# Optimization experiments

Measured on AMD Instinct MI355X. Metric: run time of the kernel, lower is better.

The kernel has to match this reference:

```python
import jax, jax.numpy as jnp
import numpy as np

# ---- static configuration (mirrors init_kwargs) ----
B, NCAM = 1, 6
FC, FH, FW = 128, 16, 44              # featureShape
ORFH, ORFW = 128, 352                 # transformedImgShape H, W
D_ST, D_END, D_STEP = 1.0, 49.0, 1.0
D = int(np.arange(D_ST, D_END, D_STEP).shape[0])   # 48 depth bins
OUTC = 128
XB = (-50.0, 50.0, 1.0)
YB = (-50.0, 50.0, 1.0)
BEV_H = int((YB[1] - YB[0]) / YB[2])  # 100
BEV_W = int((XB[1] - XB[0]) / XB[2])  # 100
THRESH = 0.05                         # opacity_filter
ERR_TOL = 1.0                         # error_tolerance
COV_DILATE = 0.3                      # 3DGS low-pass on 2D cov diagonal
ALPHA_MAX = 0.99
ALPHA_MIN = 1.0 / 255.0
BN_EPS = 1e-3


def _frustum():
    ds = jnp.arange(D_ST, D_END, D_STEP, dtype=jnp.float32)[:, None, None]
    xs = jnp.linspace(0.0, ORFW - 1.0, FW, dtype=jnp.float32)[None, None, :]
    ys = jnp.linspace(0.0, ORFH - 1.0, FH, dtype=jnp.float32)[None, :, None]
    shp = (D, FH, FW)
    return jnp.stack([jnp.broadcast_to(xs, shp), jnp.broadcast_to(ys, shp),
                      jnp.broadcast_to(ds, shp)], axis=-1)  # [D,FH,FW,3]


def _conv(x, w, b, pad):
    y = jax.lax.conv_general_dilated(x, w, (1, 1), [(pad, pad), (pad, pad)],
                                     dimension_numbers=('NCHW', 'OIHW', 'NCHW'))
    return y + b[None, :, None, None]


def _bn(x, g, beta, m, v):
    # eval-mode BatchNorm2d with running stats
    inv = g / jnp.sqrt(v + BN_EPS)
    return (x - m[None, :, None, None]) * inv[None, :, None, None] + beta[None, :, None, None]


def _rasterize(features, means, cov6, opac):
    """Differentiable BEV Gaussian splatting (alpha compositing in index order).
    features [G,C], means [G,3] (normalized to [-1,1]), cov6 [G,6]=(xx,xy,xz,yy,yz,zz), opac [G].
    """
    h, w = BEV_H, BEV_W
    sh, sw = h / 2.0, w / 2.0                 # h/FoVy, w/FoVx with FoV=2
    op = jnp.where(opac > THRESH, opac, 0.0)  # opacity cull (variable-length mask in torch)
    # full_proj_transform: row0 -> row index (y), row1 -> col index (x)
    py = h / 2.0 - sh * means[:, 1]
    px = w / 2.0 - sw * means[:, 0]
    # 2D covariance in (py,px) basis: J Sigma3 J^T with J = [[0,-sh,0],[-sw,0,0]]
    a = sh * sh * cov6[:, 3] + COV_DILATE     # var along py (from Sigma_yy)
    b = sh * sw * cov6[:, 1]                  # cov(py,px) (from Sigma_xy)
    c = sw * sw * cov6[:, 0] + COV_DILATE     # var along px (from Sigma_xx)
    det = a * c - b * b
    op = jnp.where(det > 0.0, op, 0.0)
    inv_det = 1.0 / jnp.where(det > 0.0, det, 1.0)
    ys = jnp.arange(h, dtype=jnp.float32)
    xs = jnp.arange(w, dtype=jnp.float32)
    dy = py[None, :] - ys[:, None]            # [h,G]
    dx = px[None, :] - xs[:, None]            # [w,G]
    # power = -0.5 d^T Sigma2^{-1} d, Sigma2^{-1} = [[c,-b],[-b,a]]/det
    power = (-0.5 * (c * inv_det) * dy * dy)[:, None, :] \
            + (-0.5 * (a * inv_det) * dx * dx)[None, :, :] \
            + (b * inv_det) * dy[:, None, :] * dx[None, :, :]   # [h,w,G]
    alpha = jnp.minimum(ALPHA_MAX, op * jnp.exp(jnp.minimum(power, 0.0)))
    alpha = jnp.where(alpha < ALPHA_MIN, 0.0, alpha)
    T = jnp.cumprod(1.0 - alpha, axis=-1)
    T_excl = jnp.concatenate([jnp.ones_like(T[..., :1]), T[..., :-1]], axis=-1)
    wgt = alpha * T_excl                      # [h,w,G]
    bev = jnp.einsum('hwg,gc->chw', wgt, features)   # bg color = 0
    return bev


def reference(cam2ego_rot, cam2ego_trans, cam_intrins, post_cam2ego_rot, post_cam2ego_trans,
              img_feats, conv1_w, conv1_b, bn1_g, bn1_b, bn1_m, bn1_v,
              conv2_w, conv2_b, bn2_g, bn2_b, bn2_m, bn2_v, conv3_w, conv3_b):
    # --- geometry lifting ---
    frustum = _frustum()                                             # [D,FH,FW,3]
    pts = frustum[None, None] - post_cam2ego_trans[:, :, None, None, None, :]
    pts = jnp.einsum('bnij,bndhwj->bndhwi', jnp.linalg.inv(post_cam2ego_rot), pts)
    pts = jnp.concatenate([pts[..., :2] * pts[..., 2:3], pts[..., 2:3]], axis=-1)
    combine = cam2ego_rot @ jnp.linalg.inv(cam_intrins)
    geometry = jnp.einsum('bnij,bndhwj->bndhwi', combine, pts) \
               + cam2ego_trans[:, :, None, None, None, :]            # [B,N,D,FH,FW,3]
    # --- depth net ---
    x = img_feats.reshape(B * NCAM, FC, FH, FW)
    x = jax.nn.relu(_bn(_conv(x, conv1_w, conv1_b, 1), bn1_g, bn1_b, bn1_m, bn1_v))
    x = jax.nn.relu(_bn(_conv(x, conv2_w, conv2_b, 1), bn2_g, bn2_b, bn2_m, bn2_v))
    x = _conv(x, conv3_w, conv3_b, 0)                                # [B*N, OUTC+D+1, H, W]
    depth_prob = jax.nn.softmax(x[:, :D], axis=1).reshape(B, NCAM, D, FH, FW)
    opac = jax.nn.sigmoid(x[:, D:D + 1]).reshape(B, NCAM, FH, FW)
    feats = x[:, D + 1:].reshape(B, NCAM, OUTC, FH, FW)
    # --- per-pixel Gaussian moments over the depth distribution ---
    means3d = jnp.einsum('bndhw,bndhwi->bnhwi', depth_prob, geometry)
    delta = means3d[:, :, None] - geometry                           # [B,N,D,FH,FW,3]
    cov = jnp.einsum('bndhw,bndhwi,bndhwj->bnhwij', depth_prob, delta, delta)
    cov = cov * (ERR_TOL ** 2 / 9.0)
    # --- normalize to BEV frame ---
    center = jnp.array([(XB[0] + XB[1]) / 2.0, (YB[0] + YB[1]) / 2.0, 0.0], jnp.float32)
    scale = jnp.array([2.0 / (XB[1] - XB[0]), 2.0 / (YB[1] - YB[0]), 1.0], jnp.float32)
    means_n = (means3d - center) * scale
    cov_n = cov * (scale[:, None] * scale[None, :])
    cov6 = jnp.stack([cov_n[..., 0, 0], cov_n[..., 0, 1], cov_n[..., 0, 2],
                      cov_n[..., 1, 1], cov_n[..., 1, 2], cov_n[..., 2, 2]], axis=-1)
    G = NCAM * FH * FW
    f = jnp.transpose(feats, (0, 1, 3, 4, 2)).reshape(B, G, OUTC)
    m = means_n.reshape(B, G, 3)
    c6 = cov6.reshape(B, G, 6)
    o = opac.reshape(B, G)
    bev = jax.vmap(_rasterize)(f, m, c6, o)                          # [B,OUTC,BEV_H,BEV_W]
    return bev


def setup_inputs() -> dict:
    key = jax.random.key(0)
    ks = jax.random.split(key, 16)
    eye = jnp.eye(3, dtype=jnp.float32)
    cam2ego_rot = eye + 0.05 * jax.random.normal(ks[0], (B, NCAM, 3, 3), jnp.float32)
    cam2ego_trans = 0.5 * jax.random.normal(ks[1], (B, NCAM, 3), jnp.float32)
    intr = jnp.array([[260.0, 0.0, ORFW / 2.0], [0.0, 260.0, ORFH / 2.0], [0.0, 0.0, 1.0]], jnp.float32)
    cam_intrins = jnp.broadcast_to(intr, (B, NCAM, 3, 3)) * (1.0 + 0.01 * jax.random.normal(ks[2], (B, NCAM, 1, 1), jnp.float32))
    post_cam2ego_rot = eye + 0.01 * jax.random.normal(ks[3], (B, NCAM, 3, 3), jnp.float32)
    post_cam2ego_trans = 2.0 * jax.random.normal(ks[4], (B, NCAM, 3), jnp.float32)
    img_feats = jax.random.normal(ks[5], (B, NCAM, FC, FH, FW), jnp.float32)
    def cw(k, o, i, kh, kw):
        return jax.random.normal(k, (o, i, kh, kw), jnp.float32) / np.sqrt(i * kh * kw)
    inp = dict(cam2ego_rot=cam2ego_rot, cam2ego_trans=cam2ego_trans, cam_intrins=cam_intrins,
               post_cam2ego_rot=post_cam2ego_rot, post_cam2ego_trans=post_cam2ego_trans,
               img_feats=img_feats,
               conv1_w=cw(ks[6], FC, FC, 3, 3), conv1_b=jnp.zeros((FC,), jnp.float32),
               bn1_g=jnp.ones((FC,), jnp.float32), bn1_b=0.1 * jax.random.normal(ks[7], (FC,), jnp.float32),
               bn1_m=jnp.zeros((FC,), jnp.float32), bn1_v=jnp.ones((FC,), jnp.float32),
               conv2_w=cw(ks[8], FC, FC, 3, 3), conv2_b=jnp.zeros((FC,), jnp.float32),
               bn2_g=jnp.ones((FC,), jnp.float32), bn2_b=0.1 * jax.random.normal(ks[9], (FC,), jnp.float32),
               bn2_m=jnp.zeros((FC,), jnp.float32), bn2_v=jnp.ones((FC,), jnp.float32),
               conv3_w=cw(ks[10], OUTC + D + 1, FC, 1, 1),
               conv3_b=jnp.zeros((OUTC + D + 1,), jnp.float32))
    return inp
```

## Files before the change

kernel.cpp:

```cpp
#include <hip/hip_runtime.h>
#include <math.h>

#define NCAM 6
#define FHh 16
#define FWw 44
#define PIX 704
#define FCc 128
#define DB 48
#define C3 177
#define C3PAD 192
#define KCONV 1152
#define NG 4224
#define BEVN 10000
#define NSPLIT 3
#define SG 1408
#define TH_LOG (-5.5412635f)

#define OFF_WT1    0
#define OFF_WT2    147456
#define OFF_WT3    294912
#define OFF_GEO    319488
#define OFF_X1     724992
#define OFF_X2     1265664
#define OFF_X3     1806336
#define OFF_PART   2553984
#define OFF_PRM    4716672
#define OFF_PRM2   4733568
#define OFF_FEATT  4742016
#define OFF_SF     0
#define OFF_SP     3840000

typedef __attribute__((ext_vector_type(8))) short bf16x8;
typedef __attribute__((ext_vector_type(4))) float f32x4;
typedef __attribute__((ext_vector_type(4))) int i32x4;

__device__ __forceinline__ unsigned short f2bf(float x) {
  unsigned u = __float_as_uint(x);
  return (unsigned short)((u + 0x7FFF + ((u >> 16) & 1)) >> 16);
}
__device__ __forceinline__ float bf2f(unsigned short h) {
  return __uint_as_float(((unsigned)h) << 16);
}

__device__ __forceinline__ void inv3(const float* A, float* I) {
  float a=A[0],b=A[1],c=A[2],d=A[3],e=A[4],f=A[5],g=A[6],h=A[7],i=A[8];
  float c0 = e*i - f*h, c1 = f*g - d*i, c2 = d*h - e*g;
  float det = a*c0 + b*c1 + c*c2;
  float id = 1.f/det;
  I[0]=c0*id; I[1]=(c*h-b*i)*id; I[2]=(b*f-c*e)*id;
  I[3]=c1*id; I[4]=(a*i-c*g)*id; I[5]=(c*d-a*f)*id;
  I[6]=c2*id; I[7]=(b*g-a*h)*id; I[8]=(a*e-b*d)*id;
}

__global__ void k_prep(const float* __restrict__ rot, const float* __restrict__ intr,
                       const float* __restrict__ post_rot,
                       const float* __restrict__ trans, const float* __restrict__ post_trans,
                       const float* __restrict__ w1, const float* __restrict__ w2,
                       const float* __restrict__ w3, float* __restrict__ ws) {
  if (blockIdx.x < 792) {
    __shared__ float sm[NCAM][24];
    if (threadIdx.x < NCAM) {
      int n = threadIdx.x;
      float ip[9], ii[9];
      inv3(post_rot + n*9, ip);
      inv3(intr + n*9, ii);
      const float* R = rot + n*9;
      for (int j = 0; j < 9; ++j) sm[n][j] = ip[j];
      for (int r = 0; r < 3; ++r)
        for (int c = 0; c < 3; ++c) {
          float s = 0.f;
          for (int k = 0; k < 3; ++k) s += R[r*3+k]*ii[k*3+c];
          sm[n][9 + r*3 + c] = s;
        }
    }
    __syncthreads();
    int idx = blockIdx.x*256 + threadIdx.x;
    if (idx >= NCAM*DB*PIX) return;
    int n = idx / (DB*PIX);
    int rem = idx % (DB*PIX);
    int d = rem / PIX;
    int hw = rem % PIX;
    int h = hw / FWw, w = hw % FWw;
    float fx = w * (351.0f/43.0f);
    float fy = h * (127.0f/15.0f);
    float fz = 1.0f + (float)d;
    const float* pt = post_trans + n*3;
    float v0 = fx - pt[0], v1 = fy - pt[1], v2 = fz - pt[2];
    const float* m = sm[n];
    float x = m[0]*v0 + m[1]*v1 + m[2]*v2;
    float y = m[3]*v0 + m[4]*v1 + m[5]*v2;
    float z = m[6]*v0 + m[7]*v1 + m[8]*v2;
    float q0 = x*z, q1 = y*z, q2 = z;
    const float* c = m + 9;
    const float* t = trans + n*3;
    float gx = c[0]*q0 + c[1]*q1 + c[2]*q2 + t[0];
    float gy = c[3]*q0 + c[4]*q1 + c[5]*q2 + t[1];
    ((float2*)(ws + OFF_GEO))[idx] = make_float2(gx, gy);
  } else {
    int e = (blockIdx.x - 792)*256 + threadIdx.x;
    if (e < 147456) {
      float v1 = w1[e], v2 = w2[e];
      unsigned short h1 = f2bf(v1), h2 = f2bf(v2);
      unsigned short l1 = f2bf(v1 - bf2f(h1)), l2 = f2bf(v2 - bf2f(h2));
      unsigned short* wt1 = (unsigned short*)(ws + OFF_WT1);
      unsigned short* wt2 = (unsigned short*)(ws + OFF_WT2);
      wt1[e] = h1; wt1[147456 + e] = l1;
      wt2[e] = h2; wt2[147456 + e] = l2;
    }
    if (e < 192*128) {
      int oc = e >> 7, k = e & 127;
      float v = (oc < C3) ? w3[oc*FCc + k] : 0.f;
      unsigned short h = f2bf(v);
      unsigned short* wt3 = (unsigned short*)(ws + OFF_WT3);
      wt3[e] = h; wt3[24576 + e] = f2bf(v - bf2f(h));
    }
  }
}

#define LROW 20

__global__ __launch_bounds__(256) void k_gemm_mfma(
    const float* __restrict__ in, const float* ws, float* __restrict__ part, int woff)
{
  __shared__ int alds[2][64*LROW];
  __shared__ int blds[2][64*LROW];
  int tid = threadIdx.x;
  int px0 = blockIdx.x * 64;
  int oc0 = blockIdx.y * 64;
  int z = blockIdx.z; int n = z >> 2, ks = z & 3;
  const unsigned short* whi = (const unsigned short*)(ws + woff);
  const unsigned short* wlo = whi + 147456;
  const float* inn = in + (size_t)n*FCc*PIX;
  int wv = tid >> 6, lane = tid & 63;
  int a_oc = tid >> 2, a_kq = tid & 3;
  int b_px = tid & 63, b_kq = tid >> 6;
  int p = px0 + b_px; int b_y = p / FWw, b_x = p - b_y*FWw;
  int k00 = ks * 288;

  i32x4 pa_h, pa_l; float bv[8];
  auto issueA = [&](int s) {
    size_t gi = (size_t)(oc0 + a_oc)*KCONV + (k00 + s*32 + a_kq*8);
    pa_h = *(const i32x4*)(whi + gi);
    pa_l = *(const i32x4*)(wlo + gi);
  };
  auto issueB = [&](int s) {
    #pragma unroll
    for (int j = 0; j < 8; ++j) {
      int k = k00 + s*32 + b_kq*8 + j;
      int ic = k / 9, tap = k - ic*9;
      int ky = tap / 3, kx = tap - ky*3;
      int yy = b_y + ky - 1, xx = b_x + kx - 1;
      float v = 0.f;
      if ((unsigned)yy < FHh && (unsigned)xx < FWw) v = inn[(size_t)ic*PIX + yy*FWw + xx];
      bv[j] = v;
    }
  };

  f32x4 a00 = {0.f,0.f,0.f,0.f}, a01 = a00, a10 = a00, a11 = a00;
  int ocr = (wv >> 1) * 32, pxr = (wv & 1) * 32;
  int dq = (lane >> 4) * 4;
  int rA0 = (ocr + (lane & 15)) * LROW + dq;
  int rA1 = rA0 + 16*LROW;
  int rB0 = (pxr + (lane & 15)) * LROW + dq;
  int rB1 = rB0 + 16*LROW;
  int aw = a_oc*LROW + a_kq*4;
  int bw = b_px*LROW + b_kq*4;

  issueA(0); issueB(0);
  for (int s = 0; s < 9; ++s) {
    __syncthreads();
    *(i32x4*)&alds[0][aw] = pa_h;
    *(i32x4*)&alds[1][aw] = pa_l;
    {
      i32x4 vh, vl;
      int th[8], tl[8];
      #pragma unroll
      for (int j = 0; j < 8; ++j) {
        unsigned short h = f2bf(bv[j]);
        th[j] = h; tl[j] = f2bf(bv[j] - bf2f(h));
      }
      vh.x = th[0]|(th[1]<<16); vh.y = th[2]|(th[3]<<16);
      vh.z = th[4]|(th[5]<<16); vh.w = th[6]|(th[7]<<16);
      vl.x = tl[0]|(tl[1]<<16); vl.y = tl[2]|(tl[3]<<16);
      vl.z = tl[4]|(tl[5]<<16); vl.w = tl[6]|(tl[7]<<16);
      *(i32x4*)&blds[0][bw] = vh;
      *(i32x4*)&blds[1][bw] = vl;
    }
    __syncthreads();
    if (s < 8) { issueA(s+1); issueB(s+1); }
    bf16x8 ah0 = *(bf16x8*)&alds[0][rA0], ah1 = *(bf16x8*)&alds[0][rA1];
    bf16x8 al0 = *(bf16x8*)&alds[1][rA0], al1 = *(bf16x8*)&alds[1][rA1];
    bf16x8 bh0 = *(bf16x8*)&blds[0][rB0], bh1 = *(bf16x8*)&blds[0][rB1];
    bf16x8 bl0 = *(bf16x8*)&blds[1][rB0], bl1 = *(bf16x8*)&blds[1][rB1];
    a00 = __builtin_amdgcn_mfma_f32_16x16x32_bf16(ah0, bh0, a00, 0, 0, 0);
    a01 = __builtin_amdgcn_mfma_f32_16x16x32_bf16(ah0, bh1, a01, 0, 0, 0);
    a10 = __builtin_amdgcn_mfma_f32_16x16x32_bf16(ah1, bh0, a10, 0, 0, 0);
    a11 = __builtin_amdgcn_mfma_f32_16x16x32_bf16(ah1, bh1, a11, 0, 0, 0);
    a00 = __builtin_amdgcn_mfma_f32_16x16x32_bf16(ah0, bl0, a00, 0, 0, 0);
    a01 = __builtin_amdgcn_mfma_f32_16x16x32_bf16(ah0, bl1, a01, 0, 0, 0);
    a10 = __builtin_amdgcn_mfma_f32_16x16x32_bf16(ah1, bl0, a10, 0, 0, 0);
    a11 = __builtin_amdgcn_mfma_f32_16x16x32_bf16(ah1, bl1, a11, 0, 0, 0);
    a00 = __builtin_amdgcn_mfma_f32_16x16x32_bf16(al0, bh0, a00, 0, 0, 0);
    a01 = __builtin_amdgcn_mfma_f32_16x16x32_bf16(al0, bh1, a01, 0, 0, 0);
    a10 = __builtin_amdgcn_mfma_f32_16x16x32_bf16(al1, bh0, a10, 0, 0, 0);
    a11 = __builtin_amdgcn_mfma_f32_16x16x32_bf16(al1, bh1, a11, 0, 0, 0);
  }
  float* pp = part + (size_t)(ks*NCAM + n)*FCc*PIX;
  int ocb = oc0 + ocr + ((lane >> 4) << 2);
  int pxb = px0 + pxr + (lane & 15);
  #pragma unroll
  for (int i = 0; i < 4; ++i) {
    pp[(size_t)(ocb + i)*PIX + pxb]           = a00[i];
    pp[(size_t)(ocb + i)*PIX + pxb + 16]      = a01[i];
    pp[(size_t)(ocb + 16 + i)*PIX + pxb]      = a10[i];
    pp[(size_t)(ocb + 16 + i)*PIX + pxb + 16] = a11[i];
  }
}

__global__ __launch_bounds__(256) void k_gemm_mfma3(
    const float* __restrict__ in, const float* ws,
    const float* __restrict__ bias, float* __restrict__ outbuf)
{
  __shared__ int alds[2][64*LROW];
  __shared__ int blds[2][64*LROW];
  int tid = threadIdx.x;
  int px0 = blockIdx.x * 64;
  int oc0 = blockIdx.y * 64;
  int n = blockIdx.z;
  const unsigned short* whi = (const unsigned short*)(ws + OFF_WT3);
  const unsigned short* wlo = whi + 24576;
  const float* inn = in + (size_t)n*FCc*PIX;
  int wv = tid >> 6, lane = tid & 63;
  int a_oc = tid >> 2, a_kq = tid & 3;
  int b_px = tid & 63, b_kq = tid >> 6;
  int p = px0 + b_px;

  i32x4 pa_h, pa_l; float bvv[8];
  auto issueA = [&](int s) {
    size_t gi = (size_t)(oc0 + a_oc)*128 + (s*32 + a_kq*8);
    pa_h = *(const i32x4*)(whi + gi);
    pa_l = *(const i32x4*)(wlo + gi);
  };
  auto issueB = [&](int s) {
    #pragma unroll
    for (int j = 0; j < 8; ++j) {
      int ic = s*32 + b_kq*8 + j;
      bvv[j] = inn[(size_t)ic*PIX + p];
    }
  };

  f32x4 a00 = {0.f,0.f,0.f,0.f}, a01 = a00, a10 = a00, a11 = a00;
  int ocr = (wv >> 1) * 32, pxr = (wv & 1) * 32;
  int dq = (lane >> 4) * 4;
  int rA0 = (ocr + (lane & 15)) * LROW + dq;
  int rA1 = rA0 + 16*LROW;
  int rB0 = (pxr + (lane & 15)) * LROW + dq;
  int rB1 = rB0 + 16*LROW;
  int aw = a_oc*LROW + a_kq*4;
  int bw = b_px*LROW + b_kq*4;

  issueA(0); issueB(0);
  for (int s = 0; s < 4; ++s) {
    __syncthreads();
    *(i32x4*)&alds[0][aw] = pa_h;
    *(i32x4*)&alds[1][aw] = pa_l;
    {
      i32x4 vh, vl;
      int th[8], tl[8];
      #pragma unroll
      for (int j = 0; j < 8; ++j) {
        unsigned short h = f2bf(bvv[j]);
        th[j] = h; tl[j] = f2bf(bvv[j] - bf2f(h));
      }
      vh.x = th[0]|(th[1]<<16); vh.y = th[2]|(th[3]<<16);
      vh.z = th[4]|(th[5]<<16); vh.w = th[6]|(th[7]<<16);
      vl.x = tl[0]|(tl[1]<<16); vl.y = tl[2]|(tl[3]<<16);
      vl.z = tl[4]|(tl[5]<<16); vl.w = tl[6]|(tl[7]<<16);
      *(i32x4*)&blds[0][bw] = vh;
      *(i32x4*)&blds[1][bw] = vl;
    }
    __syncthreads();
    if (s < 3) { issueA(s+1); issueB(s+1); }
    bf16x8 ah0 = *(bf16x8*)&alds[0][rA0], ah1 = *(bf16x8*)&alds[0][rA1];
    bf16x8 al0 = *(bf16x8*)&alds[1][rA0], al1 = *(bf16x8*)&alds[1][rA1];
    bf16x8 bh0 = *(bf16x8*)&blds[0][rB0], bh1 = *(bf16x8*)&blds[0][rB1];
    bf16x8 bl0 = *(bf16x8*)&blds[1][rB0], bl1 = *(bf16x8*)&blds[1][rB1];
    a00 = __builtin_amdgcn_mfma_f32_16x16x32_bf16(ah0, bh0, a00, 0, 0, 0);
    a01 = __builtin_amdgcn_mfma_f32_16x16x32_bf16(ah0, bh1, a01, 0, 0, 0);
    a10 = __builtin_amdgcn_mfma_f32_16x16x32_bf16(ah1, bh0, a10, 0, 0, 0);
    a11 = __builtin_amdgcn_mfma_f32_16x16x32_bf16(ah1, bh1, a11, 0, 0, 0);
    a00 = __builtin_amdgcn_mfma_f32_16x16x32_bf16(ah0, bl0, a00, 0, 0, 0);
    a01 = __builtin_amdgcn_mfma_f32_16x16x32_bf16(ah0, bl1, a01, 0, 0, 0);
    a10 = __builtin_amdgcn_mfma_f32_16x16x32_bf16(ah1, bl0, a10, 0, 0, 0);
    a11 = __builtin_amdgcn_mfma_f32_16x16x32_bf16(ah1, bl1, a11, 0, 0, 0);
    a00 = __builtin_amdgcn_mfma_f32_16x16x32_bf16(al0, bh0, a00, 0, 0, 0);
    a01 = __builtin_amdgcn_mfma_f32_16x16x32_bf16(al0, bh1, a01, 0, 0, 0);
    a10 = __builtin_amdgcn_mfma_f32_16x16x32_bf16(al1, bh0, a10, 0, 0, 0);
    a11 = __builtin_amdgcn_mfma_f32_16x16x32_bf16(al1, bh1, a11, 0, 0, 0);
  }
  int ocb = oc0 + ocr + ((lane >> 4) << 2);
  int pxb = px0 + pxr + (lane & 15);
  #pragma unroll
  for (int i = 0; i < 4; ++i) {
    int o0 = ocb + i, o1 = ocb + 16 + i;
    if (o0 < C3) {
      float b = bias[o0];
      outbuf[(size_t)(n*C3 + o0)*PIX + pxb]      = a00[i] + b;
      outbuf[(size_t)(n*C3 + o0)*PIX + pxb + 16] = a01[i] + b;
    }
    if (o1 < C3) {
      float b = bias[o1];
      outbuf[(size_t)(n*C3 + o1)*PIX + pxb]      = a10[i] + b;
      outbuf[(size_t)(n*C3 + o1)*PIX + pxb + 16] = a11[i] + b;
    }
  }
}

__global__ void k_epi_bn(const float* __restrict__ part, const float* __restrict__ cb,
                         const float* __restrict__ g, const float* __restrict__ be,
                         const float* __restrict__ mn, const float* __restrict__ vr,
                         float* __restrict__ out, int KSPLIT)
{
  int idx = blockIdx.x*256 + threadIdx.x;
  if (idx >= NCAM*FCc*176) return;
  int px4 = idx % 176;
  int t = idx / 176;
  int oc = t % FCc;
  int n = t / FCc;
  float4 s = {0.f,0.f,0.f,0.f};
  for (int ks = 0; ks < KSPLIT; ++ks) {
    const float4* p = (const float4*)(part + (size_t)((ks*NCAM+n)*FCc + oc)*PIX);
    float4 v = p[px4];
    s.x += v.x; s.y += v.y; s.z += v.z; s.w += v.w;
  }
  float inv = g[oc] * rsqrtf(vr[oc] + 1e-3f);
  float sh = (cb[oc] - mn[oc]) * inv + be[oc];
  float4 o;
  o.x = fmaxf(s.x*inv + sh, 0.f);
  o.y = fmaxf(s.y*inv + sh, 0.f);
  o.z = fmaxf(s.z*inv + sh, 0.f);
  o.w = fmaxf(s.w*inv + sh, 0.f);
  ((float4*)(out + (size_t)(n*FCc + oc)*PIX))[px4] = o;
}

__global__ void k_moments(float* __restrict__ ws) {
  int wid  = (blockIdx.x * 256 + threadIdx.x) >> 6;
  int lane = threadIdx.x & 63;
  int n = wid / PIX, hw = wid % PIX;
  const float* x3 = ws + OFF_X3 + (size_t)n*C3*PIX + hw;
  float logit = (lane < DB) ? x3[(size_t)lane*PIX] : -1e30f;
  float mx = logit;
  for (int off = 1; off < 64; off <<= 1) mx = fmaxf(mx, __shfl_xor(mx, off));
  float e = (lane < DB) ? expf(logit - mx) : 0.f;
  float s = e;
  for (int off = 1; off < 64; off <<= 1) s += __shfl_xor(s, off);
  float p = e / s;
  float gx = 0.f, gy = 0.f;
  if (lane < DB) {
    float2 g2 = ((const float2*)(ws + OFF_GEO))[(size_t)(n*DB + lane)*PIX + hw];
    gx = g2.x; gy = g2.y;
  }
  float sx = p*gx;
  for (int off = 1; off < 64; off <<= 1) sx += __shfl_xor(sx, off);
  float sy = p*gy;
  for (int off = 1; off < 64; off <<= 1) sy += __shfl_xor(sy, off);
  float dx = gx - sx, dy = gy - sy;
  float c00 = p*dx*dx, c01 = p*dx*dy, c11 = p*dy*dy;
  for (int off = 1; off < 64; off <<= 1) c00 += __shfl_xor(c00, off);
  for (int off = 1; off < 64; off <<= 1) c01 += __shfl_xor(c01, off);
  for (int off = 1; off < 64; off <<= 1) c11 += __shfl_xor(c11, off);
  float opl = x3[(size_t)DB*PIX];
  float opac = 1.f / (1.f + expf(-opl));
  float a = c11*(1.f/9.f) + 0.3f;
  float b = c01*(1.f/9.f);
  float c = c00*(1.f/9.f) + 0.3f;
  float py = 50.f - sy;
  float px = 50.f - sx;
  float det = a*c - b*b;
  float op = (opac > 0.05f) ? opac : 0.f;
  float invd = 1.f;
  if (det > 0.f) invd = 1.f/det; else op = 0.f;
  if (lane == 0) {
    float lop = (op > 0.f) ? logf(op) : -1e30f;
    ((float4*)(ws + OFF_PRM))[wid]  = make_float4(py, px, -0.5f*c*invd, -0.5f*a*invd);
    ((float2*)(ws + OFF_PRM2))[wid] = make_float2(b*invd, lop);
  }
  unsigned lo = f2bf(x3[(size_t)(DB + 1 + 2*lane)*PIX]);
  unsigned hi = f2bf(x3[(size_t)(DB + 1 + 2*lane + 1)*PIX]);
  ((unsigned*)(ws + OFF_FEATT))[(size_t)wid*64 + lane] = lo | (hi << 16);
}

template<int CTRL, int RMASK>
__device__ __forceinline__ float dpp_mul(float v) {
  int t = __builtin_amdgcn_update_dpp(0x3f800000, __float_as_int(v), CTRL, RMASK, 0xF, false);
  return v * __int_as_float(t);
}

__global__ __launch_bounds__(1024) void k_raster(const float* __restrict__ ws,
                                                 float* __restrict__ wsout) {
  __shared__ float4 s4[SG];
  __shared__ float2 s2[SG];
  int lane = threadIdx.x & 63, wv = threadIdx.x >> 6;
  int split = blockIdx.x / 625;
  int pxb   = blockIdx.x % 625;
  int pix = pxb * 16 + wv;
  float yi = (float)(pix / 100), xi = (float)(pix % 100);
  int gbase = split * SG;
  const float4* prm4 = (const float4*)(ws + OFF_PRM) + gbase;
  const float2* prm2 = (const float2*)(ws + OFF_PRM2) + gbase;
  const unsigned* ftu = (const unsigned*)(ws + OFF_FEATT);
  for (int i = threadIdx.x; i < SG; i += 1024) {
    s4[i] = prm4[i];
    s2[i] = prm2[i];
  }
  __syncthreads();
  float T = 1.f, ax = 0.f, ay = 0.f;
  for (int gl = 0; gl < SG; gl += 64) {
    float4 c4 = s4[gl + lane];
    float2 c2 = s2[gl + lane];
    float dyv = c4.x - yi, dxv = c4.y - xi;
    float pw = c4.z*dyv*dyv + c4.w*dxv*dxv + c2.x*dyv*dxv;
    float t  = pw + c2.y;
    bool hit = (t >= TH_LOG);
    unsigned long long m0 = __ballot(hit);
    if (m0) {
      float alpha = __expf(fminf(t, c2.y));
      alpha = fminf(alpha, 0.99f);
      alpha = hit ? alpha : 0.f;
      float P = 1.f - alpha;
      P = dpp_mul<0x111, 0xF>(P);
      P = dpp_mul<0x112, 0xF>(P);
      P = dpp_mul<0x114, 0xF>(P);
      P = dpp_mul<0x118, 0xF>(P);
      P = dpp_mul<0x142, 0xA>(P);
      P = dpp_mul<0x143, 0xC>(P);
      float E = __int_as_float(__builtin_amdgcn_update_dpp(
                  0x3f800000, __float_as_int(P), 0x138, 0xF, 0xF, false));
      float w = alpha * T * E;
      T *= __int_as_float(__builtin_amdgcn_readlane(__float_as_int(P), 63));
      unsigned long long mask = __ballot(w > 1e-9f);
      int g0 = gbase + gl;
      while (mask) {
        int jj[8];
        #pragma unroll
        for (int b = 0; b < 8; ++b) {
          if (mask) { jj[b] = __builtin_ctzll(mask); mask &= mask - 1ull; }
          else jj[b] = -1;
        }
        unsigned ub[8]; float wb[8];
        #pragma unroll
        for (int b = 0; b < 8; ++b) {
          int j = (jj[b] >= 0) ? jj[b] : jj[0];
          ub[b] = ftu[(size_t)(g0 + j)*64 + lane];
          wb[b] = (jj[b] >= 0)
            ? __int_as_float(__builtin_amdgcn_readlane(__float_as_int(w), jj[b]))
            : 0.f;
        }
        #pragma unroll
        for (int b = 0; b < 8; ++b) {
          ax += wb[b]*bf2f((unsigned short)(ub[b] & 0xffff));
          ay += wb[b]*bf2f((unsigned short)(ub[b] >> 16));
        }
      }
      if (T < 1e-7f) break;
    }
  }
  float* sf = wsout + OFF_SF + ((size_t)split*BEVN + pix)*128;
  sf[2*lane]   = ax;
  sf[2*lane+1] = ay;
  if (lane == 0) (wsout + OFF_SP)[split*BEVN + pix] = T;
}

__global__ __launch_bounds__(512) void k_combine(const float* __restrict__ ws,
                                                 float* __restrict__ out) {
  int lane = threadIdx.x & 63, wv = threadIdx.x >> 6;
  int pix = blockIdx.x * 8 + wv;
  const float* sp = ws + OFF_SP;
  float P0 = sp[pix], P1 = sp[BEVN + pix];
  const float2* f0 = (const float2*)(ws + OFF_SF + (size_t)pix*128);
  const float2* f1 = (const float2*)(ws + OFF_SF + ((size_t)BEVN + pix)*128);
  const float2* f2 = (const float2*)(ws + OFF_SF + ((size_t)2*BEVN + pix)*128);
  float2 a = f0[lane], b = f1[lane], c = f2[lane];
  float w1 = P0, w2 = P0*P1;
  float ox = a.x + w1*b.x + w2*c.x;
  float oy = a.y + w1*b.y + w2*c.y;
  out[(size_t)(2*lane)*BEVN + pix]   = ox;
  out[(size_t)(2*lane+1)*BEVN + pix] = oy;
}

extern "C" void kernel_launch(void* const* d_in, const int* in_sizes, int n_in,
                              void* d_out, int out_size, void* d_ws, size_t ws_size,
                              hipStream_t stream) {
  const float* rot        = (const float*)d_in[0];
  const float* trans      = (const float*)d_in[1];
  const float* intr       = (const float*)d_in[2];
  const float* post_rot   = (const float*)d_in[3];
  const float* post_trans = (const float*)d_in[4];
  const float* img        = (const float*)d_in[5];
  const float* w1  = (const float*)d_in[6];
  const float* b1  = (const float*)d_in[7];
  const float* g1  = (const float*)d_in[8];
  const float* be1 = (const float*)d_in[9];
  const float* m1  = (const float*)d_in[10];
  const float* v1  = (const float*)d_in[11];
  const float* w2  = (const float*)d_in[12];
  const float* b2  = (const float*)d_in[13];
  const float* g2  = (const float*)d_in[14];
  const float* be2 = (const float*)d_in[15];
  const float* m2  = (const float*)d_in[16];
  const float* v2  = (const float*)d_in[17];
  const float* w3  = (const float*)d_in[18];
  const float* b3  = (const float*)d_in[19];
  float* ws  = (float*)d_ws;
  float* out = (float*)d_out;

  k_prep<<<1368, 256, 0, stream>>>(rot, intr, post_rot, trans, post_trans,
                                   w1, w2, w3, ws);

  k_gemm_mfma<<<dim3(11,2,24), 256, 0, stream>>>(img, ws, ws+OFF_PART, OFF_WT1);
  k_epi_bn<<<528, 256, 0, stream>>>(ws+OFF_PART, b1, g1, be1, m1, v1, ws+OFF_X1, 4);
  k_gemm_mfma<<<dim3(11,2,24), 256, 0, stream>>>(ws+OFF_X1, ws, ws+OFF_PART, OFF_WT2);
  k_epi_bn<<<528, 256, 0, stream>>>(ws+OFF_PART, b2, g2, be2, m2, v2, ws+OFF_X2, 4);
  k_gemm_mfma3<<<dim3(11,3,6), 256, 0, stream>>>(ws+OFF_X2, ws, b3, ws+OFF_X3);

  k_moments<<<1056, 256, 0, stream>>>(ws);
  k_raster<<<1875, 1024, 0, stream>>>(ws, ws);
  k_combine<<<1250, 512, 0, stream>>>(ws, out);
}
```

Measured before the change: 124.6 us.

## Software-pipeline raster alpha eval and issue feature loads before the prefix product

The rasterizer now evaluates the next 64-Gaussian chunk's alpha and hit mask one iteration ahead. It issues the first batch of up to eight feature gathers, keyed on the hit mask, before computing the DPP transmittance prefix product, so memory latency overlaps ALU work. The weight-based mask (w > 1e-9) is replaced by the plain hit mask. This may load features whose contribution is negligible, and it raises register pressure.

```diff
diff --git a/kernel.cpp b/kernel.cpp
--- a/kernel.cpp
+++ b/kernel.cpp
@@ -414,20 +414,43 @@
     s2[i] = prm2[i];
   }
   __syncthreads();
-  float T = 1.f, ax = 0.f, ay = 0.f;
-  for (int gl = 0; gl < SG; gl += 64) {
+
+  auto evalA = [&](int gl, float& alpha) -> unsigned long long {
     float4 c4 = s4[gl + lane];
     float2 c2 = s2[gl + lane];
     float dyv = c4.x - yi, dxv = c4.y - xi;
     float pw = c4.z*dyv*dyv + c4.w*dxv*dxv + c2.x*dyv*dxv;
     float t  = pw + c2.y;
     bool hit = (t >= TH_LOG);
-    unsigned long long m0 = __ballot(hit);
-    if (m0) {
-      float alpha = __expf(fminf(t, c2.y));
-      alpha = fminf(alpha, 0.99f);
-      alpha = hit ? alpha : 0.f;
-      float P = 1.f - alpha;
+    float a = __expf(fminf(t, c2.y));
+    a = fminf(a, 0.99f);
+    alpha = hit ? a : 0.f;
+    return __ballot(hit);
+  };
+
+  float T = 1.f, ax = 0.f, ay = 0.f;
+  float alpha_c;
+  unsigned long long m_c = evalA(0, alpha_c);
+  for (int gl = 0; gl < SG; gl += 64) {
+    float alpha_n = 0.f;
+    unsigned long long m_n = 0ull;
+    if (gl + 64 < SG) m_n = evalA(gl + 64, alpha_n);
+    if (m_c) {
+      int g0 = gbase + gl;
+      unsigned long long mask = m_c;
+      int jj[8];
+      #pragma unroll
+      for (int b = 0; b < 8; ++b) {
+        if (mask) { jj[b] = __builtin_ctzll(mask); mask &= mask - 1ull; }
+        else jj[b] = -1;
+      }
+      unsigned ub[8];
+      #pragma unroll
+      for (int b = 0; b < 8; ++b) {
+        int j = (jj[b] >= 0) ? jj[b] : jj[0];
+        ub[b] = ftu[(size_t)(g0 + j)*64 + lane];
+      }
+      float P = 1.f - alpha_c;
       P = dpp_mul<0x111, 0xF>(P);
       P = dpp_mul<0x112, 0xF>(P);
       P = dpp_mul<0x114, 0xF>(P);
@@ -436,34 +459,41 @@
       P = dpp_mul<0x143, 0xC>(P);
       float E = __int_as_float(__builtin_amdgcn_update_dpp(
                   0x3f800000, __float_as_int(P), 0x138, 0xF, 0xF, false));
-      float w = alpha * T * E;
+      float w = alpha_c * T * E;
       T *= __int_as_float(__builtin_amdgcn_readlane(__float_as_int(P), 63));
-      unsigned long long mask = __ballot(w > 1e-9f);
-      int g0 = gbase + gl;
+      #pragma unroll
+      for (int b = 0; b < 8; ++b) {
+        float wb = (jj[b] >= 0)
+          ? __int_as_float(__builtin_amdgcn_readlane(__float_as_int(w), jj[b]))
+          : 0.f;
+        ax += wb*bf2f((unsigned short)(ub[b] & 0xffff));
+        ay += wb*bf2f((unsigned short)(ub[b] >> 16));
+      }
       while (mask) {
-        int jj[8];
+        int kk[8];
         #pragma unroll
         for (int b = 0; b < 8; ++b) {
-          if (mask) { jj[b] = __builtin_ctzll(mask); mask &= mask - 1ull; }
-          else jj[b] = -1;
+          if (mask) { kk[b] = __builtin_ctzll(mask); mask &= mask - 1ull; }
+          else kk[b] = -1;
         }
-        unsigned ub[8]; float wb[8];
+        unsigned vb[8]; float wb[8];
         #pragma unroll
         for (int b = 0; b < 8; ++b) {
-          int j = (jj[b] >= 0) ? jj[b] : jj[0];
-          ub[b] = ftu[(size_t)(g0 + j)*64 + lane];
-          wb[b] = (jj[b] >= 0)
-            ? __int_as_float(__builtin_amdgcn_readlane(__float_as_int(w), jj[b]))
+          int j = (kk[b] >= 0) ? kk[b] : kk[0];
+          vb[b] = ftu[(size_t)(g0 + j)*64 + lane];
+          wb[b] = (kk[b] >= 0)
+            ? __int_as_float(__builtin_amdgcn_readlane(__float_as_int(w), kk[b]))
             : 0.f;
         }
         #pragma unroll
         for (int b = 0; b < 8; ++b) {
-          ax += wb[b]*bf2f((unsigned short)(ub[b] & 0xffff));
-          ay += wb[b]*bf2f((unsigned short)(ub[b] >> 16));
+          ax += wb[b]*bf2f((unsigned short)(vb[b] & 0xffff));
+          ay += wb[b]*bf2f((unsigned short)(vb[b] >> 16));
         }
       }
       if (T < 1e-7f) break;
     }
+    alpha_c = alpha_n; m_c = m_n;
   }
   float* sf = wsout + OFF_SF + ((size_t)split*BEVN + pix)*128;
   sf[2*lane]   = ax;
```

After: 128.3 us. 1.03x slower.
